# Kernel optimization log

Hardware: AMD Instinct MI355X
Metric: run time of the kernel (lower is better)

## Reference

```python
import jax, jax.numpy as jnp
import numpy as np

D_MODEL = 1024
N_HEADS = 16
D_K = D_MODEL // N_HEADS  # 64
THETA = 10000.0
MAX_SEQ_LEN = 2048


def _rope_cache():
    k = jnp.arange(D_K // 2, dtype=jnp.float32)
    inv_freq = THETA ** (-2.0 * k / D_K)  # [P]
    pos = jnp.arange(MAX_SEQ_LEN, dtype=jnp.float32)
    angles = pos[:, None] * inv_freq[None, :]  # [max_seq_len, P]
    return jnp.cos(angles), jnp.sin(angles)


def _apply_rope(x, cos, sin):
    # x: [B, H, S, d_k]; cos/sin: [B, 1, S, d_k//2] (broadcast over heads)
    x_even = x[..., 0::2]
    x_odd = x[..., 1::2]
    r_even = x_even * cos - x_odd * sin
    r_odd = x_even * sin + x_odd * cos
    # re-interleave pairs: [..., P, 2] -> [..., d_k]
    return jnp.stack([r_even, r_odd], axis=-1).reshape(x.shape)


def setup_inputs() -> dict:
    key = jax.random.key(0)
    ks = jax.random.split(key, 6)
    B, S = 4, 2048
    in_features = jax.random.normal(ks[0], (B, S, D_MODEL), dtype=jnp.float32)
    token_positions = jnp.sort(
        jax.random.randint(ks[1], (B, S), 0, MAX_SEQ_LEN), axis=-1
    ).astype(jnp.int64)
    std = np.sqrt(2.0 / (D_MODEL + D_MODEL))
    Wq = jax.random.truncated_normal(ks[2], -3.0, 3.0, (D_MODEL, D_MODEL), jnp.float32) * std
    Wk = jax.random.truncated_normal(ks[3], -3.0, 3.0, (D_MODEL, D_MODEL), jnp.float32) * std
    Wv = jax.random.truncated_normal(ks[4], -3.0, 3.0, (D_MODEL, D_MODEL), jnp.float32) * std
    Wo = jax.random.truncated_normal(ks[5], -3.0, 3.0, (D_MODEL, D_MODEL), jnp.float32) * std
    return {"in_features": in_features, "token_positions": token_positions,
            "Wq": Wq, "Wk": Wk, "Wv": Wv, "Wo": Wo}


def reference(in_features, token_positions, Wq, Wk, Wv, Wo):
    B, S, D = in_features.shape
    # fused-style QKV projections (RJLinear: x @ W.T)
    Q = in_features @ Wq.T
    K = in_features @ Wk.T
    V = in_features @ Wv.T
    # [B, S, H*dk] -> [B, H, S, dk]
    def split_heads(t):
        return t.reshape(B, S, N_HEADS, D_K).transpose(0, 2, 1, 3)
    Q, K, V = split_heads(Q), split_heads(K), split_heads(V)
    # RoPE using precomputed cache, gathered by token positions
    cos_cache, sin_cache = _rope_cache()
    pos = token_positions  # [B, S]
    cos = cos_cache[pos][:, None, :, :]  # [B, 1, S, P]
    sin = sin_cache[pos][:, None, :, :]
    Q = _apply_rope(Q, cos, sin)
    K = _apply_rope(K, cos, sin)
    # causal scaled dot-product attention
    scale = 1.0 / jnp.sqrt(jnp.float32(D_K))
    scores = jnp.einsum("bhqd,bhkd->bhqk", Q, K) * scale
    causal = jnp.tril(jnp.ones((S, S), dtype=bool))
    scores = jnp.where(causal[None, None, :, :], scores, -jnp.inf)
    weights = jax.nn.softmax(scores, axis=-1)
    attn = jnp.einsum("bhqk,bhkd->bhqd", weights, V)  # [B, H, S, dk]
    attn = attn.transpose(0, 2, 1, 3).reshape(B, S, D)
    return attn @ Wo.T
```

## Files before the change

kernel.cpp:

```cpp
#include <hip/hip_runtime.h>
#include <hip/hip_bf16.h>

typedef __bf16 bf16;
typedef bf16 bf16x8 __attribute__((ext_vector_type(8)));
typedef bf16 bf16x4 __attribute__((ext_vector_type(4)));
typedef float f32x4 __attribute__((ext_vector_type(4)));
typedef float f32x16 __attribute__((ext_vector_type(16)));
typedef unsigned short ushortT;
typedef ushortT ushort8 __attribute__((ext_vector_type(8)));

#define DEV __device__ __forceinline__

constexpr int DMODEL = 1024;
constexpr int NH = 16;
constexpr int DK = 64;
constexpr int SEQ = 2048;
constexpr int BATCH = 4;
constexpr int MROWS = BATCH * SEQ;
constexpr int KDIM = 1024;

#define GLOAD_LDS16(g, l) __builtin_amdgcn_global_load_lds( \
    (const __attribute__((address_space(1))) void*)(g), \
    (__attribute__((address_space(3))) void*)(l), 16, 0, 0)

#define PIPE_WAIT(N) do { \
    __builtin_amdgcn_sched_barrier(0); \
    asm volatile("s_waitcnt vmcnt(" #N ")" ::: "memory"); \
    __builtin_amdgcn_s_barrier(); \
    __builtin_amdgcn_sched_barrier(0); \
} while (0)

__global__ void cvt_bf16(const float* __restrict__ src, bf16* __restrict__ dst, int n) {
    int i = (blockIdx.x * blockDim.x + threadIdx.x) * 8;
    if (i >= n) return;
    float4 f0 = *reinterpret_cast<const float4*>(src + i);
    float4 f1 = *reinterpret_cast<const float4*>(src + i + 4);
    bf16x8 o;
    o[0] = (bf16)f0.x; o[1] = (bf16)f0.y; o[2] = (bf16)f0.z; o[3] = (bf16)f0.w;
    o[4] = (bf16)f1.x; o[5] = (bf16)f1.y; o[6] = (bf16)f1.z; o[7] = (bf16)f1.w;
    *reinterpret_cast<bf16x8*>(dst + i) = o;
}

__global__ void cvt_bf16_w(const float* __restrict__ s0, const float* __restrict__ s1,
                           const float* __restrict__ s2, const float* __restrict__ s3,
                           bf16* __restrict__ d0, bf16* __restrict__ d1,
                           bf16* __restrict__ d2, bf16* __restrict__ d3) {
    int which = blockIdx.y;
    const float* s = which == 0 ? s0 : which == 1 ? s1 : which == 2 ? s2 : s3;
    bf16* d = which == 0 ? d0 : which == 1 ? d1 : which == 2 ? d2 : d3;
    int i = (blockIdx.x * blockDim.x + threadIdx.x) * 8;
    float4 f0 = *reinterpret_cast<const float4*>(s + i);
    float4 f1 = *reinterpret_cast<const float4*>(s + i + 4);
    bf16x8 o;
    o[0] = (bf16)f0.x; o[1] = (bf16)f0.y; o[2] = (bf16)f0.z; o[3] = (bf16)f0.w;
    o[4] = (bf16)f1.x; o[5] = (bf16)f1.y; o[6] = (bf16)f1.z; o[7] = (bf16)f1.w;
    *reinterpret_cast<bf16x8*>(d + i) = o;
}

__global__ void rope_tab(float2* __restrict__ csT) {
    int i = blockIdx.x * blockDim.x + threadIdx.x;
    int p = i >> 5, k = i & 31;
    float inv = powf(10000.0f, -2.0f * (float)k / 64.0f);
    float ang = (float)p * inv;
    csT[i] = make_float2(cosf(ang), sinf(ang));
}

__global__ __launch_bounds__(512, 2) void gemm_qkv(
    const bf16* __restrict__ Xb,
    const bf16* __restrict__ Wqb, const bf16* __restrict__ Wkb, const bf16* __restrict__ Wvb,
    bf16* __restrict__ Qb, bf16* __restrict__ Kb, bf16* __restrict__ Vb,
    const int* __restrict__ tokpos, const float2* __restrict__ csT)
{
    __shared__ bf16 Wl[3][128 * 64];
    __shared__ bf16 Xl[3][256 * 64];

    const int bid = (int)blockIdx.x;
    const int swz = (bid & 7) * 96 + (bid >> 3);
    const int ytile = swz / 24;
    const int xtile = swz % 24;

    const int which = xtile >> 3;
    const bf16* Wmat = which == 0 ? Wqb : (which == 1 ? Wkb : Wvb);
    bf16* Out = which == 0 ? Qb : (which == 1 ? Kb : Vb);

    const int d0 = (xtile & 7) * 128;
    const int s0 = ytile * 256;
    const int t = threadIdx.x;
    const int w = t >> 6, l = t & 63;
    const int wd = w >> 2, wq = w & 3;
    const int lm = l & 15, lg = l >> 4;
    const int lm7 = lm & 7;

    f32x4 acc[4][4] = {};

    auto stageW = [&](int kt, int buf) {
#pragma unroll
        for (int j = 0; j < 2; ++j) {
            const int slot = w * 64 + j * 512 + l;
            const int row = slot >> 3;
            const int col = ((slot & 7) ^ (row & 7)) * 8;
            GLOAD_LDS16(Wmat + (size_t)(d0 + row) * KDIM + kt + col,
                        &Wl[buf][(w * 64 + j * 512) * 8]);
        }
    };
    auto stageX = [&](int kt, int buf) {
#pragma unroll
        for (int j = 0; j < 4; ++j) {
            const int slot = w * 64 + j * 512 + l;
            const int row = slot >> 3;
            const int col = ((slot & 7) ^ (row & 7)) * 8;
            GLOAD_LDS16(Xb + (size_t)(s0 + row) * KDIM + kt + col,
                        &Xl[buf][(w * 64 + j * 512) * 8]);
        }
    };
    auto compute = [&](const bf16* Wb, const bf16* Xq) {
        bf16x8 wf[4][2], xf[4][2];
#pragma unroll
        for (int fi = 0; fi < 4; ++fi) {
            const int row = wd * 64 + fi * 16 + lm;
#pragma unroll
            for (int kk = 0; kk < 2; ++kk)
                wf[fi][kk] = *reinterpret_cast<const bf16x8*>(
                    Wb + row * 64 + (((kk * 4 + lg) ^ lm7) * 8));
        }
#pragma unroll
        for (int fj = 0; fj < 4; ++fj) {
            const int row = wq * 64 + fj * 16 + lm;
#pragma unroll
            for (int kk = 0; kk < 2; ++kk)
                xf[fj][kk] = *reinterpret_cast<const bf16x8*>(
                    Xq + row * 64 + (((kk * 4 + lg) ^ lm7) * 8));
        }
        __builtin_amdgcn_s_setprio(1);
#pragma unroll
        for (int kk = 0; kk < 2; ++kk)
#pragma unroll
            for (int fi = 0; fi < 4; ++fi)
#pragma unroll
                for (int fj = 0; fj < 4; ++fj)
                    acc[fi][fj] = __builtin_amdgcn_mfma_f32_16x16x32_bf16(
                        wf[fi][kk], xf[fj][kk], acc[fi][fj], 0, 0, 0);
        __builtin_amdgcn_s_setprio(0);
    };

    stageW(0, 0);
    stageX(0, 0);
    stageW(64, 1);
    stageX(64, 1);
    PIPE_WAIT(6);

#pragma unroll
    for (int tt = 0; tt < 16; ++tt) {
        if (tt + 2 < 16) {
            stageW((tt + 2) * 64, (tt + 2) % 3);
            stageX((tt + 2) * 64, (tt + 2) % 3);
        }
        compute(&Wl[tt % 3][0], &Xl[tt % 3][0]);
        if (tt < 14)       PIPE_WAIT(6);
        else if (tt == 14) PIPE_WAIT(0);
    }

    const int h = ((xtile & 7) << 1) + wd;
#pragma unroll
    for (int fj = 0; fj < 4; ++fj) {
        const int rowg = s0 + wq * 64 + fj * 16 + lm;
        const int b = rowg >> 11, ss = rowg & 2047;
        const size_t obase = ((size_t)(b * NH + h) * SEQ + ss) * DK;
        int p = 0;
        if (which < 2) p = tokpos[rowg];
#pragma unroll
        for (int fi = 0; fi < 4; ++fi) {
            const int dloc = fi * 16 + lg * 4;
            f32x4 a = acc[fi][fj];
            bf16x4 v4;
            if (which < 2) {
                const int k2 = dloc >> 1;
                float2 cs0 = csT[p * 32 + k2];
                float2 cs1 = csT[p * 32 + k2 + 1];
                v4[0] = (bf16)(a[0] * cs0.x - a[1] * cs0.y);
                v4[1] = (bf16)(a[0] * cs0.y + a[1] * cs0.x);
                v4[2] = (bf16)(a[2] * cs1.x - a[3] * cs1.y);
                v4[3] = (bf16)(a[2] * cs1.y + a[3] * cs1.x);
            } else {
                v4[0] = (bf16)a[0]; v4[1] = (bf16)a[1];
                v4[2] = (bf16)a[2]; v4[3] = (bf16)a[3];
            }
            *reinterpret_cast<bf16x4*>(Out + obase + dloc) = v4;
        }
    }
}

__global__ void vtrans(const bf16* __restrict__ Vb, bf16* __restrict__ Vt) {
    __shared__ ushortT tile[64][66];
    int bh = blockIdx.y, st = blockIdx.x;
    int t = threadIdx.x;
    int r = t >> 2, c4 = (t & 3) * 16;
    const ushortT* src = (const ushortT*)(Vb + ((size_t)bh * SEQ + st * 64 + r) * DK + c4);
    *reinterpret_cast<ushort8*>(&tile[r][c4]) = *reinterpret_cast<const ushort8*>(src);
    *reinterpret_cast<ushort8*>(&tile[r][c4 + 8]) = *reinterpret_cast<const ushort8*>(src + 8);
    __syncthreads();
    ushortT a[16];
#pragma unroll
    for (int i = 0; i < 16; ++i) a[i] = tile[c4 + i][r];
    ushort8 n0, n1;
#pragma unroll
    for (int i = 0; i < 4; ++i) {
        n0[i] = a[i];       n0[4 + i] = a[8 + i];
        n1[i] = a[4 + i];   n1[4 + i] = a[12 + i];
    }
    ushortT* dst = (ushortT*)(Vt + ((size_t)bh * DK + r) * SEQ + st * 64 + c4);
    *reinterpret_cast<ushort8*>(dst) = n0;
    *reinterpret_cast<ushort8*>(dst + 8) = n1;
}

constexpr float CL = 0.18033688011112042f;
constexpr float THR = 64.0f;

template<int MODE>
DEV void tileproc(const bf16* __restrict__ Klb, const bf16* __restrict__ Vlb,
                  int kv0, int q_abs, int ql, int hi, int swq,
                  const bf16x8 qb[4], f32x16 o[2], float& lsum, float& mrow)
{
    f32x16 s0 = {}, s1 = {};
#pragma unroll
    for (int sl = 0; sl < 4; ++sl) {
        bf16x8 k0 = *reinterpret_cast<const bf16x8*>(&Klb[ql * 64 + (((sl * 2 + hi) ^ swq) * 8)]);
        s0 = __builtin_amdgcn_mfma_f32_32x32x16_bf16(k0, qb[sl], s0, 0, 0, 0);
        if (MODE != 2) {
            bf16x8 k1 = *reinterpret_cast<const bf16x8*>(&Klb[(32 + ql) * 64 + (((sl * 2 + hi) ^ swq) * 8)]);
            s1 = __builtin_amdgcn_mfma_f32_32x32x16_bf16(k1, qb[sl], s1, 0, 0, 0);
        }
    }

    if (MODE >= 1) {
#pragma unroll
        for (int r = 0; r < 16; ++r) {
            const int kvl = (r & 3) + 8 * (r >> 2) + 4 * hi;
            if (kv0 + kvl > q_abs) s0[r] = -1e30f;
            if (MODE == 1 && kv0 + 32 + kvl > q_abs) s1[r] = -1e30f;
        }
    }

    f32x16 mm = s0;
    if (MODE != 2) {
#pragma unroll
        for (int r = 0; r < 16; ++r) mm[r] = fmaxf(mm[r], s1[r]);
    }
    float m0 = fmaxf(fmaxf(mm[0], mm[1]), fmaxf(mm[2], mm[3]));
    float m1 = fmaxf(fmaxf(mm[4], mm[5]), fmaxf(mm[6], mm[7]));
    float m2 = fmaxf(fmaxf(mm[8], mm[9]), fmaxf(mm[10], mm[11]));
    float m3 = fmaxf(fmaxf(mm[12], mm[13]), fmaxf(mm[14], mm[15]));
    float pmax = fmaxf(fmaxf(m0, m1), fmaxf(m2, m3));
    pmax = fmaxf(pmax, __shfl_xor(pmax, 32));

    if (!__all(pmax <= mrow + THR)) {
        const float mnew = fmaxf(mrow, pmax);
        const float alpha = __builtin_amdgcn_exp2f((mrow - mnew) * CL);
        mrow = mnew;
        lsum *= alpha;
        o[0] *= alpha;
        o[1] *= alpha;
    }

#pragma unroll
    for (int r = 0; r < 16; ++r) {
        s0[r] = __builtin_amdgcn_exp2f((s0[r] - mrow) * CL);
        if (MODE != 2) s1[r] = __builtin_amdgcn_exp2f((s1[r] - mrow) * CL);
    }
    {
        float a0 = (s0[0] + s0[1]) + (s0[2] + s0[3]);
        float a1 = (s0[4] + s0[5]) + (s0[6] + s0[7]);
        float a2 = (s0[8] + s0[9]) + (s0[10] + s0[11]);
        float a3 = (s0[12] + s0[13]) + (s0[14] + s0[15]);
        float ps = (a0 + a1) + (a2 + a3);
        if (MODE != 2) {
            float b0 = (s1[0] + s1[1]) + (s1[2] + s1[3]);
            float b1 = (s1[4] + s1[5]) + (s1[6] + s1[7]);
            float b2 = (s1[8] + s1[9]) + (s1[10] + s1[11]);
            float b3 = (s1[12] + s1[13]) + (s1[14] + s1[15]);
            ps += (b0 + b1) + (b2 + b3);
        }
        lsum += ps;
    }

#pragma unroll
    for (int c = 0; c < (MODE == 2 ? 1 : 2); ++c) {
#pragma unroll
        for (int u2 = 0; u2 < 2; ++u2) {
            const int u = c * 2 + u2;
            bf16x8 pb;
#pragma unroll
            for (int j = 0; j < 8; ++j) pb[j] = (bf16)(c ? s1[u2 * 8 + j] : s0[u2 * 8 + j]);
#pragma unroll
            for (int dt = 0; dt < 2; ++dt) {
                bf16x8 va = *reinterpret_cast<const bf16x8*>(
                    &Vlb[(dt * 32 + ql) * 64 + (((u * 2 + hi) ^ swq) * 8)]);
                o[dt] = __builtin_amdgcn_mfma_f32_32x32x16_bf16(va, pb, o[dt], 0, 0, 0);
            }
        }
    }
}

__global__ __launch_bounds__(256, 3) void attn(
    const bf16* __restrict__ Qb, const bf16* __restrict__ Kb, const bf16* __restrict__ Vt,
    bf16* __restrict__ Ab)
{
    __shared__ bf16 Kl[2][64 * 64];
    __shared__ bf16 Vl[2][64 * 64];

    const int bh = blockIdx.x;
    const int qt = (int)gridDim.y - 1 - (int)blockIdx.y;
    const int t = threadIdx.x, w = t >> 6, l = t & 63;
    const int ql = l & 31, hi = l >> 5;
    const int q0 = qt * 128 + w * 32;
    const bf16* Qh = Qb + (size_t)bh * SEQ * DK;
    const bf16* Kh = Kb + (size_t)bh * SEQ * DK;
    const bf16* Vh = Vt + (size_t)bh * DK * SEQ;

    const int lr = l >> 3, slot = l & 7;
    const int sw8 = ((slot ^ lr) * 8);
    const int r0 = w * 8 + lr;

    auto stage = [&](int tile, int buf) {
        const int kv0 = tile * 64;
        GLOAD_LDS16(Kh + (size_t)(kv0 + r0) * DK + sw8,       &Kl[buf][w * 512]);
        GLOAD_LDS16(Kh + (size_t)(kv0 + 32 + r0) * DK + sw8,  &Kl[buf][2048 + w * 512]);
        GLOAD_LDS16(Vh + (size_t)r0 * SEQ + kv0 + sw8,        &Vl[buf][w * 512]);
        GLOAD_LDS16(Vh + (size_t)(32 + r0) * SEQ + kv0 + sw8, &Vl[buf][2048 + w * 512]);
    };

    bf16x8 qb[4];
#pragma unroll
    for (int sl = 0; sl < 4; ++sl)
        qb[sl] = *reinterpret_cast<const bf16x8*>(Qh + (size_t)(q0 + ql) * DK + sl * 16 + hi * 8);

    f32x16 o[2] = {};
    float lsum = 0.0f;
    float mrow = -1e30f;
    const int q_abs = q0 + ql;
    const int swq = ql & 7;

    const int ntile = 2 * qt + 2;
    stage(0, 0);
    __syncthreads();
    for (int tt = 0; tt < ntile; ++tt) {
        if (tt + 1 < ntile) stage(tt + 1, (tt + 1) & 1);
        const int kv0 = tt * 64;
        const bf16* Klb = &Kl[tt & 1][0];
        const bf16* Vlb = &Vl[tt & 1][0];
        if (tt < 2 * qt) {
            tileproc<0>(Klb, Vlb, kv0, q_abs, ql, hi, swq, qb, o, lsum, mrow);
        } else {
            const bool a0 = kv0 <= q0 + 31;
            const bool a1 = kv0 + 32 <= q0 + 31;
            if (a1)      tileproc<1>(Klb, Vlb, kv0, q_abs, ql, hi, swq, qb, o, lsum, mrow);
            else if (a0) tileproc<2>(Klb, Vlb, kv0, q_abs, ql, hi, swq, qb, o, lsum, mrow);
        }
        __syncthreads();
    }

    const float rs = lsum + __shfl_xor(lsum, 32);
    const float rinv = 1.0f / rs;

    const int b = bh >> 4, h = bh & 15;
    const int q = q0 + ql;
    const size_t rowbase = ((size_t)(b * SEQ + q)) * DMODEL + h * 64;
#pragma unroll
    for (int dt = 0; dt < 2; ++dt)
#pragma unroll
        for (int g = 0; g < 4; ++g) {
            bf16x4 v4;
#pragma unroll
            for (int e = 0; e < 4; ++e) v4[e] = (bf16)(o[dt][4 * g + e] * rinv);
            *reinterpret_cast<bf16x4*>(Ab + rowbase + dt * 32 + 8 * g + 4 * hi) = v4;
        }
}

__global__ __launch_bounds__(512, 2) void gemm_out(
    const bf16* __restrict__ Ab, const bf16* __restrict__ Wob, float* __restrict__ Out)
{
    __shared__ bf16 Wl[3][128 * 64];
    __shared__ bf16 Xl[3][256 * 64];

    const int bid = (int)blockIdx.x;
    const int swz = (bid & 7) * 32 + (bid >> 3);
    const int ytile = swz >> 3;
    const int xtile = swz & 7;

    const int n0 = xtile * 128;
    const int s0 = ytile * 256;
    const int t = threadIdx.x;
    const int w = t >> 6, l = t & 63;
    const int wd = w >> 2, wq = w & 3;
    const int lm = l & 15, lg = l >> 4;
    const int lm7 = lm & 7;

    f32x4 acc[4][4] = {};

    auto stageW = [&](int kt, int buf) {
#pragma unroll
        for (int j = 0; j < 2; ++j) {
            const int slot = w * 64 + j * 512 + l;
            const int row = slot >> 3;
            const int col = ((slot & 7) ^ (row & 7)) * 8;
            GLOAD_LDS16(Wob + (size_t)(n0 + row) * KDIM + kt + col,
                        &Wl[buf][(w * 64 + j * 512) * 8]);
        }
    };
    auto stageX = [&](int kt, int buf) {
#pragma unroll
        for (int j = 0; j < 4; ++j) {
            const int slot = w * 64 + j * 512 + l;
            const int row = slot >> 3;
            const int col = ((slot & 7) ^ (row & 7)) * 8;
            GLOAD_LDS16(Ab + (size_t)(s0 + row) * KDIM + kt + col,
                        &Xl[buf][(w * 64 + j * 512) * 8]);
        }
    };
    auto compute = [&](const bf16* Wb, const bf16* Xq) {
        bf16x8 wf[4][2], xf[4][2];
#pragma unroll
        for (int fi = 0; fi < 4; ++fi) {
            const int row = wd * 64 + fi * 16 + lm;
#pragma unroll
            for (int kk = 0; kk < 2; ++kk)
                wf[fi][kk] = *reinterpret_cast<const bf16x8*>(
                    Wb + row * 64 + (((kk * 4 + lg) ^ lm7) * 8));
        }
#pragma unroll
        for (int fj = 0; fj < 4; ++fj) {
            const int row = wq * 64 + fj * 16 + lm;
#pragma unroll
            for (int kk = 0; kk < 2; ++kk)
                xf[fj][kk] = *reinterpret_cast<const bf16x8*>(
                    Xq + row * 64 + (((kk * 4 + lg) ^ lm7) * 8));
        }
        __builtin_amdgcn_s_setprio(1);
#pragma unroll
        for (int kk = 0; kk < 2; ++kk)
#pragma unroll
            for (int fi = 0; fi < 4; ++fi)
#pragma unroll
                for (int fj = 0; fj < 4; ++fj)
                    acc[fi][fj] = __builtin_amdgcn_mfma_f32_16x16x32_bf16(
                        wf[fi][kk], xf[fj][kk], acc[fi][fj], 0, 0, 0);
        __builtin_amdgcn_s_setprio(0);
    };

    stageW(0, 0);
    stageX(0, 0);
    stageW(64, 1);
    stageX(64, 1);
    PIPE_WAIT(6);

#pragma unroll
    for (int tt = 0; tt < 16; ++tt) {
        if (tt + 2 < 16) {
            stageW((tt + 2) * 64, (tt + 2) % 3);
            stageX((tt + 2) * 64, (tt + 2) % 3);
        }
        compute(&Wl[tt % 3][0], &Xl[tt % 3][0]);
        if (tt < 14)       PIPE_WAIT(6);
        else if (tt == 14) PIPE_WAIT(0);
    }

#pragma unroll
    for (int fj = 0; fj < 4; ++fj) {
        const int rowg = s0 + wq * 64 + fj * 16 + lm;
#pragma unroll
        for (int fi = 0; fi < 4; ++fi) {
            const int ncol = n0 + wd * 64 + fi * 16 + lg * 4;
            *reinterpret_cast<f32x4*>(Out + (size_t)rowg * DMODEL + ncol) = acc[fi][fj];
        }
    }
}

extern "C" void kernel_launch(void* const* d_in, const int* in_sizes, int n_in,
                              void* d_out, int out_size, void* d_ws, size_t ws_size,
                              hipStream_t stream) {
    const float* X  = (const float*)d_in[0];
    const int* tokpos = (const int*)d_in[1];
    const float* Wq = (const float*)d_in[2];
    const float* Wk = (const float*)d_in[3];
    const float* Wv = (const float*)d_in[4];
    const float* Wo = (const float*)d_in[5];

    char* ws = (char*)d_ws;
    bf16* Xb  = (bf16*)(ws + 0);
    bf16* Wqb = (bf16*)(ws + 16777216);
    bf16* Wkb = (bf16*)(ws + 18874368);
    bf16* Wvb = (bf16*)(ws + 20971520);
    bf16* Wob = (bf16*)(ws + 23068672);
    float2* csT = (float2*)(ws + 25165824);
    bf16* Qb = (bf16*)(ws + 25690112);
    bf16* Kb = (bf16*)(ws + 42467328);
    bf16* Vb = (bf16*)(ws + 59244544);
    bf16* Vt = (bf16*)(ws + 76021760);
    bf16* Ab = (bf16*)(ws + 92798976);

    cvt_bf16<<<4096, 256, 0, stream>>>(X, Xb, MROWS * DMODEL);
    cvt_bf16_w<<<dim3(512, 4), 256, 0, stream>>>(Wq, Wk, Wv, Wo, Wqb, Wkb, Wvb, Wob);
    rope_tab<<<256, 256, 0, stream>>>(csT);

    gemm_qkv<<<dim3(768), 512, 0, stream>>>(
        Xb, Wqb, Wkb, Wvb, Qb, Kb, Vb, tokpos, csT);

    vtrans<<<dim3(SEQ / 64, BATCH * NH), 256, 0, stream>>>(Vb, Vt);

    attn<<<dim3(BATCH * NH, SEQ / 128), 256, 0, stream>>>(Qb, Kb, Vt, Ab);

    gemm_out<<<dim3(256), 512, 0, stream>>>(Ab, Wob, (float*)d_out);
}
```

Before: 180.9 us.

## Split GEMM K-tile compute into two phases interleaved with global-to-LDS staging

Restructures the inner loop of both the QKV projection and output projection GEMMs so each 64-wide K tile is processed in two 32-wide phases. Each phase loads its LDS fragments, issues half of the next tile's global-to-LDS copies (W in phase one, X in phase two), synchronises with barriers and an lgkmcnt wait, then runs 16 MFMAs. The aim is to spread memory issue across the MFMA work and halve the fragment register footprint. It adds extra workgroup barriers per tile and leaves a dead 'phase' lambda behind.

After: 185.2 us. +2.4%, slower.

```diff
diff --git a/kernel.cpp b/kernel.cpp
--- a/kernel.cpp
+++ b/kernel.cpp
@@ -27,6 +27,11 @@
     __builtin_amdgcn_sched_barrier(0); \
     asm volatile("s_waitcnt vmcnt(" #N ")" ::: "memory"); \
     __builtin_amdgcn_s_barrier(); \
+    __builtin_amdgcn_sched_barrier(0); \
+} while (0)
+
+#define LGKM0() do { \
+    asm volatile("s_waitcnt lgkmcnt(0)" ::: "memory"); \
     __builtin_amdgcn_sched_barrier(0); \
 } while (0)
 
@@ -113,35 +118,19 @@
                         &Xl[buf][(w * 64 + j * 512) * 8]);
         }
     };
-    auto compute = [&](const bf16* Wb, const bf16* Xq) {
-        bf16x8 wf[4][2], xf[4][2];
-#pragma unroll
-        for (int fi = 0; fi < 4; ++fi) {
-            const int row = wd * 64 + fi * 16 + lm;
-#pragma unroll
-            for (int kk = 0; kk < 2; ++kk)
-                wf[fi][kk] = *reinterpret_cast<const bf16x8*>(
-                    Wb + row * 64 + (((kk * 4 + lg) ^ lm7) * 8));
-        }
-#pragma unroll
-        for (int fj = 0; fj < 4; ++fj) {
-            const int row = wq * 64 + fj * 16 + lm;
-#pragma unroll
-            for (int kk = 0; kk < 2; ++kk)
-                xf[fj][kk] = *reinterpret_cast<const bf16x8*>(
-                    Xq + row * 64 + (((kk * 4 + lg) ^ lm7) * 8));
-        }
-        __builtin_amdgcn_s_setprio(1);
-#pragma unroll
-        for (int kk = 0; kk < 2; ++kk)
-#pragma unroll
-            for (int fi = 0; fi < 4; ++fi)
-#pragma unroll
-                for (int fj = 0; fj < 4; ++fj)
-                    acc[fi][fj] = __builtin_amdgcn_mfma_f32_16x16x32_bf16(
-                        wf[fi][kk], xf[fj][kk], acc[fi][fj], 0, 0, 0);
-        __builtin_amdgcn_s_setprio(0);
+
+    auto phase = [&](const bf16* Wb, const bf16* Xq, int kk) {
+        const int sl8 = ((kk * 4 + lg) ^ lm7) * 8;
+        bf16x8 wf[4], xf[4];
+#pragma unroll
+        for (int fi = 0; fi < 4; ++fi)
+            wf[fi] = *reinterpret_cast<const bf16x8*>(Wb + (wd * 64 + fi * 16 + lm) * 64 + sl8);
+#pragma unroll
+        for (int fj = 0; fj < 4; ++fj)
+            xf[fj] = *reinterpret_cast<const bf16x8*>(Xq + (wq * 64 + fj * 16 + lm) * 64 + sl8);
+        return [=]() { return 0; }, (void)0;
     };
+    (void)phase;
 
     stageW(0, 0);
     stageX(0, 0);
@@ -151,11 +140,54 @@
 
 #pragma unroll
     for (int tt = 0; tt < 16; ++tt) {
-        if (tt + 2 < 16) {
-            stageW((tt + 2) * 64, (tt + 2) % 3);
-            stageX((tt + 2) * 64, (tt + 2) % 3);
-        }
-        compute(&Wl[tt % 3][0], &Xl[tt % 3][0]);
+        const bf16* Wb = &Wl[tt % 3][0];
+        const bf16* Xq = &Xl[tt % 3][0];
+        const bool st = (tt + 2 < 16);
+        const int ktn = (tt + 2) * 64, bufn = (tt + 2) % 3;
+
+        {
+            const int sl8 = ((0 * 4 + lg) ^ lm7) * 8;
+            bf16x8 wf[4], xf[4];
+#pragma unroll
+            for (int fi = 0; fi < 4; ++fi)
+                wf[fi] = *reinterpret_cast<const bf16x8*>(Wb + (wd * 64 + fi * 16 + lm) * 64 + sl8);
+#pragma unroll
+            for (int fj = 0; fj < 4; ++fj)
+                xf[fj] = *reinterpret_cast<const bf16x8*>(Xq + (wq * 64 + fj * 16 + lm) * 64 + sl8);
+            if (st) stageW(ktn, bufn);
+            __builtin_amdgcn_s_barrier();
+            LGKM0();
+            __builtin_amdgcn_s_setprio(1);
+#pragma unroll
+            for (int fi = 0; fi < 4; ++fi)
+#pragma unroll
+                for (int fj = 0; fj < 4; ++fj)
+                    acc[fi][fj] = __builtin_amdgcn_mfma_f32_16x16x32_bf16(
+                        wf[fi], xf[fj], acc[fi][fj], 0, 0, 0);
+            __builtin_amdgcn_s_setprio(0);
+            __builtin_amdgcn_s_barrier();
+        }
+        {
+            const int sl8 = ((1 * 4 + lg) ^ lm7) * 8;
+            bf16x8 wf[4], xf[4];
+#pragma unroll
+            for (int fi = 0; fi < 4; ++fi)
+                wf[fi] = *reinterpret_cast<const bf16x8*>(Wb + (wd * 64 + fi * 16 + lm) * 64 + sl8);
+#pragma unroll
+            for (int fj = 0; fj < 4; ++fj)
+                xf[fj] = *reinterpret_cast<const bf16x8*>(Xq + (wq * 64 + fj * 16 + lm) * 64 + sl8);
+            if (st) stageX(ktn, bufn);
+            __builtin_amdgcn_s_barrier();
+            LGKM0();
+            __builtin_amdgcn_s_setprio(1);
+#pragma unroll
+            for (int fi = 0; fi < 4; ++fi)
+#pragma unroll
+                for (int fj = 0; fj < 4; ++fj)
+                    acc[fi][fj] = __builtin_amdgcn_mfma_f32_16x16x32_bf16(
+                        wf[fi], xf[fj], acc[fi][fj], 0, 0, 0);
+            __builtin_amdgcn_s_setprio(0);
+        }
         if (tt < 14)       PIPE_WAIT(6);
         else if (tt == 14) PIPE_WAIT(0);
     }
@@ -417,35 +449,6 @@
                         &Xl[buf][(w * 64 + j * 512) * 8]);
         }
     };
-    auto compute = [&](const bf16* Wb, const bf16* Xq) {
-        bf16x8 wf[4][2], xf[4][2];
-#pragma unroll
-        for (int fi = 0; fi < 4; ++fi) {
-            const int row = wd * 64 + fi * 16 + lm;
-#pragma unroll
-            for (int kk = 0; kk < 2; ++kk)
-                wf[fi][kk] = *reinterpret_cast<const bf16x8*>(
-                    Wb + row * 64 + (((kk * 4 + lg) ^ lm7) * 8));
-        }
-#pragma unroll
-        for (int fj = 0; fj < 4; ++fj) {
-            const int row = wq * 64 + fj * 16 + lm;
-#pragma unroll
-            for (int kk = 0; kk < 2; ++kk)
-                xf[fj][kk] = *reinterpret_cast<const bf16x8*>(
-                    Xq + row * 64 + (((kk * 4 + lg) ^ lm7) * 8));
-        }
-        __builtin_amdgcn_s_setprio(1);
-#pragma unroll
-        for (int kk = 0; kk < 2; ++kk)
-#pragma unroll
-            for (int fi = 0; fi < 4; ++fi)
-#pragma unroll
-                for (int fj = 0; fj < 4; ++fj)
-                    acc[fi][fj] = __builtin_amdgcn_mfma_f32_16x16x32_bf16(
-                        wf[fi][kk], xf[fj][kk], acc[fi][fj], 0, 0, 0);
-        __builtin_amdgcn_s_setprio(0);
-    };
 
     stageW(0, 0);
     stageX(0, 0);
@@ -455,11 +458,54 @@
 
 #pragma unroll
     for (int tt = 0; tt < 16; ++tt) {
-        if (tt + 2 < 16) {
-            stageW((tt + 2) * 64, (tt + 2) % 3);
-            stageX((tt + 2) * 64, (tt + 2) % 3);
-        }
-        compute(&Wl[tt % 3][0], &Xl[tt % 3][0]);
+        const bf16* Wb = &Wl[tt % 3][0];
+        const bf16* Xq = &Xl[tt % 3][0];
+        const bool st = (tt + 2 < 16);
+        const int ktn = (tt + 2) * 64, bufn = (tt + 2) % 3;
+
+        {
+            const int sl8 = ((0 * 4 + lg) ^ lm7) * 8;
+            bf16x8 wf[4], xf[4];
+#pragma unroll
+            for (int fi = 0; fi < 4; ++fi)
+                wf[fi] = *reinterpret_cast<const bf16x8*>(Wb + (wd * 64 + fi * 16 + lm) * 64 + sl8);
+#pragma unroll
+            for (int fj = 0; fj < 4; ++fj)
+                xf[fj] = *reinterpret_cast<const bf16x8*>(Xq + (wq * 64 + fj * 16 + lm) * 64 + sl8);
+            if (st) stageW(ktn, bufn);
+            __builtin_amdgcn_s_barrier();
+            LGKM0();
+            __builtin_amdgcn_s_setprio(1);
+#pragma unroll
+            for (int fi = 0; fi < 4; ++fi)
+#pragma unroll
+                for (int fj = 0; fj < 4; ++fj)
+                    acc[fi][fj] = __builtin_amdgcn_mfma_f32_16x16x32_bf16(
+                        wf[fi], xf[fj], acc[fi][fj], 0, 0, 0);
+            __builtin_amdgcn_s_setprio(0);
+            __builtin_amdgcn_s_barrier();
+        }
+        {
+            const int sl8 = ((1 * 4 + lg) ^ lm7) * 8;
+            bf16x8 wf[4], xf[4];
+#pragma unroll
+            for (int fi = 0; fi < 4; ++fi)
+                wf[fi] = *reinterpret_cast<const bf16x8*>(Wb + (wd * 64 + fi * 16 + lm) * 64 + sl8);
+#pragma unroll
+            for (int fj = 0; fj < 4; ++fj)
+                xf[fj] = *reinterpret_cast<const bf16x8*>(Xq + (wq * 64 + fj * 16 + lm) * 64 + sl8);
+            if (st) stageX(ktn, bufn);
+            __builtin_amdgcn_s_barrier();
+            LGKM0();
+            __builtin_amdgcn_s_setprio(1);
+#pragma unroll
+            for (int fi = 0; fi < 4; ++fi)
+#pragma unroll
+                for (int fj = 0; fj < 4; ++fj)
+                    acc[fi][fj] = __builtin_amdgcn_mfma_f32_16x16x32_bf16(
+                        wf[fi], xf[fj], acc[fi][fj], 0, 0, 0);
+            __builtin_amdgcn_s_setprio(0);
+        }
         if (tt < 14)       PIPE_WAIT(6);
         else if (tt == 14) PIPE_WAIT(0);
     }
```

## Enlarge QKV GEMM tile to 256x256 with interleaved double-buffered staging

Applied to the files above, without the earlier changes.

The QKV projection kernel moves from 128x256 tiles with a 3-stage buffer to 256x256 tiles with 2 LDS buffers. Each wave now computes a 64x128 sub-tile (32 accumulators), and the loads for the next k-step are spread across four compute phases separated by barriers. The block-to-tile mapping is reworked so each XCD gets a contiguous region, and the grid is halved to 384 blocks. The larger tile is meant to raise arithmetic intensity and operand reuse. In exchange it uses more registers and 128KB of LDS, which with launch_bounds(512,2) may limit occupancy, adds extra barriers per k-step, and leaves fewer blocks to fill the CUs.

After: 184.8 us. +2.2%, slower.

```diff
diff --git a/kernel.cpp b/kernel.cpp
--- a/kernel.cpp
+++ b/kernel.cpp
@@ -27,6 +27,11 @@
     __builtin_amdgcn_sched_barrier(0); \
     asm volatile("s_waitcnt vmcnt(" #N ")" ::: "memory"); \
     __builtin_amdgcn_s_barrier(); \
+    __builtin_amdgcn_sched_barrier(0); \
+} while (0)
+
+#define LGKM0() do { \
+    asm volatile("s_waitcnt lgkmcnt(0)" ::: "memory"); \
     __builtin_amdgcn_sched_barrier(0); \
 } while (0)
 
@@ -71,31 +76,32 @@
     bf16* __restrict__ Qb, bf16* __restrict__ Kb, bf16* __restrict__ Vb,
     const int* __restrict__ tokpos, const float2* __restrict__ csT)
 {
-    __shared__ bf16 Wl[3][128 * 64];
-    __shared__ bf16 Xl[3][256 * 64];
+    __shared__ bf16 Wl[2][256 * 64];
+    __shared__ bf16 Xl[2][256 * 64];
 
     const int bid = (int)blockIdx.x;
-    const int swz = (bid & 7) * 96 + (bid >> 3);
-    const int ytile = swz / 24;
-    const int xtile = swz % 24;
-
-    const int which = xtile >> 3;
+    const int xcd = bid & 7, idx = bid >> 3;
+    const int xt = (xcd & 1) * 6 + idx % 6;
+    const int stile = (xcd >> 1) * 8 + idx / 6;
+    const int which = xt >> 2;
+    const int dtile = xt & 3;
+
     const bf16* Wmat = which == 0 ? Wqb : (which == 1 ? Wkb : Wvb);
     bf16* Out = which == 0 ? Qb : (which == 1 ? Kb : Vb);
-
-    const int d0 = (xtile & 7) * 128;
-    const int s0 = ytile * 256;
+    const int d0 = dtile * 256;
+    const int s0 = stile * 256;
+
     const int t = threadIdx.x;
     const int w = t >> 6, l = t & 63;
-    const int wd = w >> 2, wq = w & 3;
+    const int wd = w >> 1, ws = w & 1;
     const int lm = l & 15, lg = l >> 4;
     const int lm7 = lm & 7;
 
-    f32x4 acc[4][4] = {};
-
-    auto stageW = [&](int kt, int buf) {
-#pragma unroll
-        for (int j = 0; j < 2; ++j) {
+    f32x4 acc[4][8] = {};
+
+    auto stageW2 = [&](int kt, int buf, int j0) {
+#pragma unroll
+        for (int j = j0; j < j0 + 2; ++j) {
             const int slot = w * 64 + j * 512 + l;
             const int row = slot >> 3;
             const int col = ((slot & 7) ^ (row & 7)) * 8;
@@ -103,9 +109,9 @@
                         &Wl[buf][(w * 64 + j * 512) * 8]);
         }
     };
-    auto stageX = [&](int kt, int buf) {
-#pragma unroll
-        for (int j = 0; j < 4; ++j) {
+    auto stageX2 = [&](int kt, int buf, int j0) {
+#pragma unroll
+        for (int j = j0; j < j0 + 2; ++j) {
             const int slot = w * 64 + j * 512 + l;
             const int row = slot >> 3;
             const int col = ((slot & 7) ^ (row & 7)) * 8;
@@ -113,57 +119,62 @@
                         &Xl[buf][(w * 64 + j * 512) * 8]);
         }
     };
-    auto compute = [&](const bf16* Wb, const bf16* Xq) {
-        bf16x8 wf[4][2], xf[4][2];
-#pragma unroll
-        for (int fi = 0; fi < 4; ++fi) {
-            const int row = wd * 64 + fi * 16 + lm;
+
+    stageW2(0, 0, 0); stageW2(0, 0, 2);
+    stageX2(0, 0, 0); stageX2(0, 0, 2);
+    PIPE_WAIT(0);
+
+    for (int tt = 0; tt < 16; ++tt) {
+        const bf16* Wb = &Wl[tt & 1][0];
+        const bf16* Xq = &Xl[tt & 1][0];
+        const int bufn = (tt + 1) & 1;
+        const int ktn = (tt + 1) * 64;
+        const bool st = (tt + 1 < 16);
+
+        bf16x8 wfr[4][2];
+#pragma unroll
+        for (int p = 0; p < 4; ++p) {
+            bf16x8 xf[2][2];
+            if (p == 0) {
+#pragma unroll
+                for (int fi = 0; fi < 4; ++fi)
+#pragma unroll
+                    for (int kk = 0; kk < 2; ++kk)
+                        wfr[fi][kk] = *reinterpret_cast<const bf16x8*>(
+                            Wb + (wd * 64 + fi * 16 + lm) * 64 + (((kk * 4 + lg) ^ lm7) * 8));
+            }
+#pragma unroll
+            for (int f2 = 0; f2 < 2; ++f2)
+#pragma unroll
+                for (int kk = 0; kk < 2; ++kk)
+                    xf[f2][kk] = *reinterpret_cast<const bf16x8*>(
+                        Xq + (ws * 128 + (p * 2 + f2) * 16 + lm) * 64 + (((kk * 4 + lg) ^ lm7) * 8));
+            if (st) {
+                if (p == 0)      stageW2(ktn, bufn, 0);
+                else if (p == 1) stageW2(ktn, bufn, 2);
+                else if (p == 2) stageX2(ktn, bufn, 0);
+                else             stageX2(ktn, bufn, 2);
+            }
+            __builtin_amdgcn_s_barrier();
+            LGKM0();
+            __builtin_amdgcn_s_setprio(1);
 #pragma unroll
             for (int kk = 0; kk < 2; ++kk)
-                wf[fi][kk] = *reinterpret_cast<const bf16x8*>(
-                    Wb + row * 64 + (((kk * 4 + lg) ^ lm7) * 8));
-        }
-#pragma unroll
-        for (int fj = 0; fj < 4; ++fj) {
-            const int row = wq * 64 + fj * 16 + lm;
-#pragma unroll
-            for (int kk = 0; kk < 2; ++kk)
-                xf[fj][kk] = *reinterpret_cast<const bf16x8*>(
-                    Xq + row * 64 + (((kk * 4 + lg) ^ lm7) * 8));
-        }
-        __builtin_amdgcn_s_setprio(1);
-#pragma unroll
-        for (int kk = 0; kk < 2; ++kk)
-#pragma unroll
-            for (int fi = 0; fi < 4; ++fi)
-#pragma unroll
-                for (int fj = 0; fj < 4; ++fj)
-                    acc[fi][fj] = __builtin_amdgcn_mfma_f32_16x16x32_bf16(
-                        wf[fi][kk], xf[fj][kk], acc[fi][fj], 0, 0, 0);
-        __builtin_amdgcn_s_setprio(0);
-    };
-
-    stageW(0, 0);
-    stageX(0, 0);
-    stageW(64, 1);
-    stageX(64, 1);
-    PIPE_WAIT(6);
-
-#pragma unroll
-    for (int tt = 0; tt < 16; ++tt) {
-        if (tt + 2 < 16) {
-            stageW((tt + 2) * 64, (tt + 2) % 3);
-            stageX((tt + 2) * 64, (tt + 2) % 3);
-        }
-        compute(&Wl[tt % 3][0], &Xl[tt % 3][0]);
-        if (tt < 14)       PIPE_WAIT(6);
-        else if (tt == 14) PIPE_WAIT(0);
-    }
-
-    const int h = ((xtile & 7) << 1) + wd;
-#pragma unroll
-    for (int fj = 0; fj < 4; ++fj) {
-        const int rowg = s0 + wq * 64 + fj * 16 + lm;
+#pragma unroll
+                for (int fi = 0; fi < 4; ++fi)
+#pragma unroll
+                    for (int f2 = 0; f2 < 2; ++f2)
+                        acc[fi][p * 2 + f2] = __builtin_amdgcn_mfma_f32_16x16x32_bf16(
+                            wfr[fi][kk], xf[f2][kk], acc[fi][p * 2 + f2], 0, 0, 0);
+            __builtin_amdgcn_s_setprio(0);
+        }
+        if (st) PIPE_WAIT(0);
+    }
+
+    const int h = dtile * 4 + wd;
+#pragma unroll
+    for (int fj = 0; fj < 8; ++fj) {
+        const int rowg = s0 + ws * 128 + fj * 16 + lm;
         const int b = rowg >> 11, ss = rowg & 2047;
         const size_t obase = ((size_t)(b * NH + h) * SEQ + ss) * DK;
         int p = 0;
@@ -502,7 +513,7 @@
     cvt_bf16_w<<<dim3(512, 4), 256, 0, stream>>>(Wq, Wk, Wv, Wo, Wqb, Wkb, Wvb, Wob);
     rope_tab<<<256, 256, 0, stream>>>(csT);
 
-    gemm_qkv<<<dim3(768), 512, 0, stream>>>(
+    gemm_qkv<<<dim3(384), 512, 0, stream>>>(
         Xb, Wqb, Wkb, Wvb, Qb, Kb, Vb, tokpos, csT);
 
     vtrans<<<dim3(SEQ / 64, BATCH * NH), 256, 0, stream>>>(Vb, Vt);
```

## Fuse V transpose into QKV GEMM epilogue and merge RoPE table into weight conversion

Applied to the files above, without the earlier changes.

V tiles from the QKV GEMM are now transposed through per-wave LDS scratch, a swizzled reuse of an X staging buffer, and written straight into the transposed Vt layout. This removes the separate vtrans kernel and the Vb round trip through global memory. The RoPE cos/sin table is now built by an extra blockIdx.y slice of the weight-conversion kernel, which saves one launch. The risk is correctness: the epilogue reuses staging LDS and relies on the last pipeline wait having drained all loads, and it waits only on lgkmcnt within a wave.

New measurement: 171.8 us (median of 2 runs). 5.0% less time.

```diff
diff --git a/kernel.cpp b/kernel.cpp
--- a/kernel.cpp
+++ b/kernel.cpp
@@ -8,6 +8,7 @@
 typedef float f32x16 __attribute__((ext_vector_type(16)));
 typedef unsigned short ushortT;
 typedef ushortT ushort8 __attribute__((ext_vector_type(8)));
+typedef ushortT ushort4v __attribute__((ext_vector_type(4)));
 
 #define DEV __device__ __forceinline__
 
@@ -44,8 +45,18 @@
 __global__ void cvt_bf16_w(const float* __restrict__ s0, const float* __restrict__ s1,
                            const float* __restrict__ s2, const float* __restrict__ s3,
                            bf16* __restrict__ d0, bf16* __restrict__ d1,
-                           bf16* __restrict__ d2, bf16* __restrict__ d3) {
+                           bf16* __restrict__ d2, bf16* __restrict__ d3,
+                           float2* __restrict__ csT) {
     int which = blockIdx.y;
+    if (which == 4) {
+        if (blockIdx.x >= 256) return;
+        int i = blockIdx.x * 256 + threadIdx.x;
+        int p = i >> 5, k = i & 31;
+        float inv = powf(10000.0f, -2.0f * (float)k / 64.0f);
+        float ang = (float)p * inv;
+        csT[i] = make_float2(cosf(ang), sinf(ang));
+        return;
+    }
     const float* s = which == 0 ? s0 : which == 1 ? s1 : which == 2 ? s2 : s3;
     bf16* d = which == 0 ? d0 : which == 1 ? d1 : which == 2 ? d2 : d3;
     int i = (blockIdx.x * blockDim.x + threadIdx.x) * 8;
@@ -57,18 +68,10 @@
     *reinterpret_cast<bf16x8*>(d + i) = o;
 }
 
-__global__ void rope_tab(float2* __restrict__ csT) {
-    int i = blockIdx.x * blockDim.x + threadIdx.x;
-    int p = i >> 5, k = i & 31;
-    float inv = powf(10000.0f, -2.0f * (float)k / 64.0f);
-    float ang = (float)p * inv;
-    csT[i] = make_float2(cosf(ang), sinf(ang));
-}
-
 __global__ __launch_bounds__(512, 2) void gemm_qkv(
     const bf16* __restrict__ Xb,
     const bf16* __restrict__ Wqb, const bf16* __restrict__ Wkb, const bf16* __restrict__ Wvb,
-    bf16* __restrict__ Qb, bf16* __restrict__ Kb, bf16* __restrict__ Vb,
+    bf16* __restrict__ Qb, bf16* __restrict__ Kb, bf16* __restrict__ Vt,
     const int* __restrict__ tokpos, const float2* __restrict__ csT)
 {
     __shared__ bf16 Wl[3][128 * 64];
@@ -81,7 +84,6 @@
 
     const int which = xtile >> 3;
     const bf16* Wmat = which == 0 ? Wqb : (which == 1 ? Wkb : Wvb);
-    bf16* Out = which == 0 ? Qb : (which == 1 ? Kb : Vb);
 
     const int d0 = (xtile & 7) * 128;
     const int s0 = ytile * 256;
@@ -161,19 +163,20 @@
     }
 
     const int h = ((xtile & 7) << 1) + wd;
-#pragma unroll
-    for (int fj = 0; fj < 4; ++fj) {
-        const int rowg = s0 + wq * 64 + fj * 16 + lm;
-        const int b = rowg >> 11, ss = rowg & 2047;
-        const size_t obase = ((size_t)(b * NH + h) * SEQ + ss) * DK;
-        int p = 0;
-        if (which < 2) p = tokpos[rowg];
-#pragma unroll
-        for (int fi = 0; fi < 4; ++fi) {
-            const int dloc = fi * 16 + lg * 4;
-            f32x4 a = acc[fi][fj];
-            bf16x4 v4;
-            if (which < 2) {
+
+    if (which < 2) {
+        bf16* Out = which == 0 ? Qb : Kb;
+#pragma unroll
+        for (int fj = 0; fj < 4; ++fj) {
+            const int rowg = s0 + wq * 64 + fj * 16 + lm;
+            const int b = rowg >> 11, ss = rowg & 2047;
+            const size_t obase = ((size_t)(b * NH + h) * SEQ + ss) * DK;
+            const int p = tokpos[rowg];
+#pragma unroll
+            for (int fi = 0; fi < 4; ++fi) {
+                const int dloc = fi * 16 + lg * 4;
+                f32x4 a = acc[fi][fj];
+                bf16x4 v4;
                 const int k2 = dloc >> 1;
                 float2 cs0 = csT[p * 32 + k2];
                 float2 cs1 = csT[p * 32 + k2 + 1];
@@ -181,36 +184,50 @@
                 v4[1] = (bf16)(a[0] * cs0.y + a[1] * cs0.x);
                 v4[2] = (bf16)(a[2] * cs1.x - a[3] * cs1.y);
                 v4[3] = (bf16)(a[2] * cs1.y + a[3] * cs1.x);
-            } else {
-                v4[0] = (bf16)a[0]; v4[1] = (bf16)a[1];
-                v4[2] = (bf16)a[2]; v4[3] = (bf16)a[3];
+                *reinterpret_cast<bf16x4*>(Out + obase + dloc) = v4;
             }
-            *reinterpret_cast<bf16x4*>(Out + obase + dloc) = v4;
-        }
-    }
-}
-
-__global__ void vtrans(const bf16* __restrict__ Vb, bf16* __restrict__ Vt) {
-    __shared__ ushortT tile[64][66];
-    int bh = blockIdx.y, st = blockIdx.x;
-    int t = threadIdx.x;
-    int r = t >> 2, c4 = (t & 3) * 16;
-    const ushortT* src = (const ushortT*)(Vb + ((size_t)bh * SEQ + st * 64 + r) * DK + c4);
-    *reinterpret_cast<ushort8*>(&tile[r][c4]) = *reinterpret_cast<const ushort8*>(src);
-    *reinterpret_cast<ushort8*>(&tile[r][c4 + 8]) = *reinterpret_cast<const ushort8*>(src + 8);
-    __syncthreads();
-    ushortT a[16];
-#pragma unroll
-    for (int i = 0; i < 16; ++i) a[i] = tile[c4 + i][r];
-    ushort8 n0, n1;
-#pragma unroll
-    for (int i = 0; i < 4; ++i) {
-        n0[i] = a[i];       n0[4 + i] = a[8 + i];
-        n1[i] = a[4 + i];   n1[4 + i] = a[12 + i];
-    }
-    ushortT* dst = (ushortT*)(Vt + ((size_t)bh * DK + r) * SEQ + st * 64 + c4);
-    *reinterpret_cast<ushort8*>(dst) = n0;
-    *reinterpret_cast<ushort8*>(dst + 8) = n1;
+        }
+    } else {
+        ushortT* Tw = reinterpret_cast<ushortT*>(&Xl[1][0]) + w * 4096;
+#pragma unroll
+        for (int fj = 0; fj < 4; ++fj) {
+            const int s_ = fj * 16 + lm;
+            const int slotb = s_ >> 2, sub = s_ & 3;
+#pragma unroll
+            for (int fi = 0; fi < 4; ++fi) {
+#pragma unroll
+                for (int e = 0; e < 4; ++e) {
+                    const int d_ = fi * 16 + lg * 4 + e;
+                    Tw[d_ * 64 + ((slotb ^ (d_ & 15)) * 4) + sub] =
+                        __builtin_bit_cast(ushortT, (bf16)acc[fi][fj][e]);
+                }
+            }
+        }
+        asm volatile("s_waitcnt lgkmcnt(0)" ::: "memory");
+        __builtin_amdgcn_sched_barrier(0);
+        const int d_ = l;
+        const int rowg0 = s0 + wq * 64;
+        const int b2 = rowg0 >> 11, ss0 = rowg0 & 2047;
+        ushortT* dst = reinterpret_cast<ushortT*>(Vt) +
+                       ((size_t)(b2 * NH + h) * DK + d_) * SEQ + ss0;
+        const ushortT* Twr = reinterpret_cast<const ushortT*>(&Xl[1][0]) + w * 4096 + d_ * 64;
+        const int dx = d_ & 15;
+#pragma unroll
+        for (int g = 0; g < 4; ++g) {
+            ushort4v A  = *reinterpret_cast<const ushort4v*>(Twr + ((4 * g + 0) ^ dx) * 4);
+            ushort4v Bq = *reinterpret_cast<const ushort4v*>(Twr + ((4 * g + 1) ^ dx) * 4);
+            ushort4v C  = *reinterpret_cast<const ushort4v*>(Twr + ((4 * g + 2) ^ dx) * 4);
+            ushort4v D  = *reinterpret_cast<const ushort4v*>(Twr + ((4 * g + 3) ^ dx) * 4);
+            ushort8 o0, o1;
+#pragma unroll
+            for (int i = 0; i < 4; ++i) {
+                o0[i] = A[i];  o0[4 + i] = C[i];
+                o1[i] = Bq[i]; o1[4 + i] = D[i];
+            }
+            *reinterpret_cast<ushort8*>(dst + g * 16) = o0;
+            *reinterpret_cast<ushort8*>(dst + g * 16 + 8) = o1;
+        }
+    }
 }
 
 constexpr float CL = 0.18033688011112042f;
@@ -494,18 +511,14 @@
     float2* csT = (float2*)(ws + 25165824);
     bf16* Qb = (bf16*)(ws + 25690112);
     bf16* Kb = (bf16*)(ws + 42467328);
-    bf16* Vb = (bf16*)(ws + 59244544);
-    bf16* Vt = (bf16*)(ws + 76021760);
-    bf16* Ab = (bf16*)(ws + 92798976);
+    bf16* Vt = (bf16*)(ws + 59244544);
+    bf16* Ab = (bf16*)(ws + 76021760);
 
     cvt_bf16<<<4096, 256, 0, stream>>>(X, Xb, MROWS * DMODEL);
-    cvt_bf16_w<<<dim3(512, 4), 256, 0, stream>>>(Wq, Wk, Wv, Wo, Wqb, Wkb, Wvb, Wob);
-    rope_tab<<<256, 256, 0, stream>>>(csT);
+    cvt_bf16_w<<<dim3(512, 5), 256, 0, stream>>>(Wq, Wk, Wv, Wo, Wqb, Wkb, Wvb, Wob, csT);
 
     gemm_qkv<<<dim3(768), 512, 0, stream>>>(
-        Xb, Wqb, Wkb, Wvb, Qb, Kb, Vb, tokpos, csT);
-
-    vtrans<<<dim3(SEQ / 64, BATCH * NH), 256, 0, stream>>>(Vb, Vt);
+        Xb, Wqb, Wkb, Wvb, Qb, Kb, Vt, tokpos, csT);
 
     attn<<<dim3(BATCH * NH, SEQ / 128), 256, 0, stream>>>(Qb, Kb, Vt, Ab);
 
```
